# Performance work log

Measured on AMD Instinct MI355X. Metric: run time of the kernel, lower is better.

The kernel has to match this reference:

```python
import jax, jax.numpy as jnp
import numpy as np

B = 16384
EPS = 1e-5
DIMS = [(3072, 4096), (4096, 4096), (4096, 256), (256, 16), (16, 16), (16, 10)]


def binarize(v):
    # BNN binarization with straight-through semantics (matches .data assignment in torch)
    return v + jax.lax.stop_gradient(jnp.sign(v) - v)


def blinear(x, w, b):
    # BinarizeLinear: binarize input (in_dim != 784) and weights, float bias add
    return binarize(x) @ binarize(w).T + b


def batchnorm(x, g, b):
    m = x.mean(axis=0)
    v = x.var(axis=0)
    return (x - m) * jax.lax.rsqrt(v + EPS) * g + b


def hardtanh(x):
    return jnp.clip(x, -1.0, 1.0)


def setup_inputs() -> dict:
    key = jax.random.key(0)
    ks = jax.random.split(key, 20)
    inp = {"x": jax.random.normal(ks[0], (B, 3072), dtype=jnp.float32)}
    for i, (din, dout) in enumerate(DIMS):
        inp[f"w{i}"] = jax.random.normal(ks[1 + 2 * i], (dout, din), dtype=jnp.float32) * 0.05
        inp[f"b{i}"] = jax.random.normal(ks[2 + 2 * i], (dout,), dtype=jnp.float32) * 0.01
    # BatchNorm affine params for layers after blinear 0,1,2 and final (dims 4096,4096,256,10)
    for j, d in enumerate([4096, 4096, 256, 10]):
        inp[f"g{j}"] = jnp.ones((d,), dtype=jnp.float32)
        inp[f"be{j}"] = jnp.zeros((d,), dtype=jnp.float32)
    return inp


def reference(x, w0, b0, w1, b1, w2, b2, w3, b3, w4, b4, w5, b5,
              g0, be0, g1, be1, g2, be2, g3, be3):
    h = x.reshape(-1, 3072)
    h = hardtanh(batchnorm(blinear(h, w0, b0), g0, be0))
    h = hardtanh(batchnorm(blinear(h, w1, b1), g1, be1))
    h = hardtanh(batchnorm(blinear(h, w2, b2), g2, be2))
    h = hardtanh(blinear(h, w3, b3))
    h = hardtanh(blinear(h, w4, b4))
    h = batchnorm(blinear(h, w5, b5), g3, be3)
    return jax.nn.log_softmax(h, axis=-1)
```

## Files before the change

kernel.cpp:

```cpp
#include <hip/hip_runtime.h>
#include <stdint.h>

typedef int v4i __attribute__((ext_vector_type(4)));
typedef int v8i __attribute__((ext_vector_type(8)));
typedef float v4f __attribute__((ext_vector_type(4)));
typedef short v8s __attribute__((ext_vector_type(8)));
typedef unsigned long long ull;
typedef unsigned int uint;

#define GLOAD16(g, l)                                                          \
  __builtin_amdgcn_global_load_lds(                                            \
      (const __attribute__((address_space(1))) void*)(g),                      \
      (__attribute__((address_space(3))) void*)(l), 16, 0, 0)

__device__ __forceinline__ signed char sgnf(float v) {
  return v > 0.f ? (signed char)1 : (v < 0.f ? (signed char)-1 : (signed char)0);
}
__device__ __forceinline__ uint nib(float v) {
  return v > 0.f ? 2u : (v < 0.f ? 10u : 0u);
}

__global__ void k_bin(const float4* __restrict__ in, char4* __restrict__ out, int n4) {
  int i = blockIdx.x * blockDim.x + threadIdx.x;
  int stride = gridDim.x * blockDim.x;
  for (; i < n4; i += stride) {
    float4 v = in[i];
    char4 o;
    o.x = sgnf(v.x); o.y = sgnf(v.y); o.z = sgnf(v.z); o.w = sgnf(v.w);
    out[i] = o;
  }
}

__global__ void k_binp(const float4* __restrict__ in, uint* __restrict__ out, int n8) {
  int i = blockIdx.x * blockDim.x + threadIdx.x;
  int stride = gridDim.x * blockDim.x;
  for (; i < n8; i += stride) {
    float4 a = in[i * 2], b = in[i * 2 + 1];
    out[i] = nib(a.x) | (nib(a.y) << 4) | (nib(a.z) << 8) | (nib(a.w) << 12) |
             (nib(b.x) << 16) | (nib(b.y) << 20) | (nib(b.z) << 24) | (nib(b.w) << 28);
  }
}

#define BM 128
#define BN 128

__global__ __launch_bounds__(256, 2) void k_bgemm(
    const unsigned char* __restrict__ X, const unsigned char* __restrict__ W,
    short* __restrict__ A, ull* __restrict__ S, int M, int N, int K)
{
  __shared__ __align__(16) unsigned char As[BM * 128];
  __shared__ __align__(16) unsigned char Bs[BN * 128];
  const int Kb = K >> 1;
  const int t = threadIdx.x;
  const int lane = t & 63;
  const int wave = t >> 6;
  const int wm = wave >> 1, wn = wave & 1;
  const int bm = blockIdx.y * BM, bn = blockIdx.x * BN;

  const int srow = lane >> 3;
  const int sslot = (lane & 7);

  const unsigned char* Xb0 = X + (size_t)bm * Kb;
  const unsigned char* Wb0 = W + (size_t)bn * Kb;

  v4f acc[4][4] = {};
  v8i a8[4], b8[4];
#pragma unroll
  for (int m = 0; m < 4; ++m) { a8[m] = (v8i)(0); b8[m] = (v8i)(0); }

  const int nt = K / 256;

  for (int tile = 0; tile < nt; ++tile) {
    int kb0 = tile * 128;
#pragma unroll
    for (int c = 0; c < 4; ++c) {
      int br = (wave * 4 + c) * 8;
      int row = br + srow;
      int ss = sslot ^ (row & 7);
      GLOAD16(Xb0 + (size_t)row * Kb + kb0 + ss * 16, As + br * 128);
      GLOAD16(Wb0 + (size_t)row * Kb + kb0 + ss * 16, Bs + br * 128);
    }
    __syncthreads();
#pragma unroll
    for (int kk = 0; kk < 2; ++kk) {
#pragma unroll
      for (int m = 0; m < 4; ++m) {
        int row = wm * 64 + m * 16 + (lane & 15);
        int slot = ((kk << 2) | (lane >> 4)) ^ (row & 7);
        v4i tmp = *(const v4i*)(As + row * 128 + slot * 16);
        a8[m][0] = tmp[0]; a8[m][1] = tmp[1]; a8[m][2] = tmp[2]; a8[m][3] = tmp[3];
      }
#pragma unroll
      for (int n = 0; n < 4; ++n) {
        int row = wn * 64 + n * 16 + (lane & 15);
        int slot = ((kk << 2) | (lane >> 4)) ^ (row & 7);
        v4i tmp = *(const v4i*)(Bs + row * 128 + slot * 16);
        b8[n][0] = tmp[0]; b8[n][1] = tmp[1]; b8[n][2] = tmp[2]; b8[n][3] = tmp[3];
      }
#pragma unroll
      for (int m = 0; m < 4; ++m)
#pragma unroll
        for (int n = 0; n < 4; ++n)
          acc[m][n] = __builtin_amdgcn_mfma_scale_f32_16x16x128_f8f6f4(
              a8[m], b8[n], acc[m][n], 4 , 4 ,
              0, 0x7F7F7F7Fu, 0, 0x7F7F7F7Fu);
    }
    __syncthreads();
  }

#pragma unroll
  for (int m = 0; m < 4; ++m) {
    int rbase = bm + wm * 64 + m * 16 + (lane >> 4) * 4;
#pragma unroll
    for (int n = 0; n < 4; ++n) {
      int col = bn + wn * 64 + n * 16 + (lane & 15);
#pragma unroll
      for (int r = 0; r < 4; ++r)
        A[(size_t)(rbase + r) * N + col] = (short)(int)acc[m][n][r];
    }
  }

#pragma unroll
  for (int n = 0; n < 4; ++n) {
    int s = 0, q = 0;
#pragma unroll
    for (int m = 0; m < 4; ++m)
#pragma unroll
      for (int r = 0; r < 4; ++r) {
        int v = (int)acc[m][n][r];
        s += v; q += v * v;
      }
    s += __shfl_xor(s, 16); s += __shfl_xor(s, 32);
    q += __shfl_xor(q, 16); q += __shfl_xor(q, 32);
    if ((lane >> 4) == 0) {
      int col = bn + wn * 64 + n * 16 + (lane & 15);
      atomicAdd(&S[col], (ull)(long long)s);
      atomicAdd(&S[(size_t)N + col], (ull)(long long)q);
    }
  }
}

__global__ void k_finalize(const ull* __restrict__ sums, const float* __restrict__ g,
                           int M, int N, float* __restrict__ meanf, float* __restrict__ sgf) {
  int j = blockIdx.x * blockDim.x + threadIdx.x;
  if (j >= N) return;
  double sum = (double)(long long)sums[j];
  double sumsq = (double)(long long)sums[N + j];
  double mean = sum / (double)M;
  double var = sumsq / (double)M - mean * mean;
  if (var < 0.0) var = 0.0;
  double inv = 1.0 / sqrt(var + 1e-5);
  meanf[j] = (float)mean;
  sgf[j] = (float)(inv * (double)g[j]);
}

__global__ void k_signbn_pack(const short* __restrict__ A, const float* __restrict__ meanf,
                              const float* __restrict__ sgf, const float* __restrict__ be,
                              uint* __restrict__ Xp, int total8, int nmask) {
  int i = blockIdx.x * blockDim.x + threadIdx.x;
  int stride = gridDim.x * blockDim.x;
  for (; i < total8; i += stride) {
    v8s a = *(const v8s*)(A + (size_t)i * 8);
    int c0 = (i * 8) & nmask;
    uint b = 0;
#pragma unroll
    for (int j = 0; j < 8; ++j) {
      float z = ((float)a[j] - meanf[c0 + j]) * sgf[c0 + j] + be[c0 + j];
      b |= nib(z) << (4 * j);
    }
    Xp[i] = b;
  }
}

__global__ void k_signbn(const short4* __restrict__ A4, const float* __restrict__ meanf,
                         const float* __restrict__ sgf, const float* __restrict__ be,
                         char4* __restrict__ X4, int total4, int nmask) {
  int i = blockIdx.x * blockDim.x + threadIdx.x;
  int stride = gridDim.x * blockDim.x;
  for (; i < total4; i += stride) {
    short4 a = A4[i];
    int c0 = (i * 4) & nmask;
    char4 o;
    o.x = sgnf(((float)a.x - meanf[c0    ]) * sgf[c0    ] + be[c0    ]);
    o.y = sgnf(((float)a.y - meanf[c0 + 1]) * sgf[c0 + 1] + be[c0 + 1]);
    o.z = sgnf(((float)a.z - meanf[c0 + 2]) * sgf[c0 + 2] + be[c0 + 2]);
    o.w = sgnf(((float)a.w - meanf[c0 + 3]) * sgf[c0 + 3] + be[c0 + 3]);
    X4[i] = o;
  }
}

__global__ __launch_bounds__(256) void k_tail(
    const signed char* __restrict__ X3, const signed char* __restrict__ W3,
    const signed char* __restrict__ W4, const signed char* __restrict__ W5,
    const float* __restrict__ b3, const float* __restrict__ b4,
    int* __restrict__ A5, ull* __restrict__ sums5, int M)
{
  __shared__ __align__(16) signed char sW3[16 * 256];
  __shared__ __align__(16) signed char sW4[256];
  __shared__ __align__(16) signed char sW5[160];
  __shared__ __align__(16) signed char sX[16 * 256];
  __shared__ signed char sH[16][16];
  __shared__ int bsum[10], bsq[10];
  int t = threadIdx.x;
  int rowBlock = blockIdx.x * 16;
  ((int4*)sW3)[t] = ((const int4*)W3)[t];
  ((int4*)sX)[t] = ((const int4*)(X3 + (size_t)rowBlock * 256))[t];
  if (t < 16) ((int4*)sW4)[t] = ((const int4*)W4)[t];
  if (t < 10) {
    ((int4*)sW5)[t] = ((const int4*)W5)[t];
    bsum[t] = 0; bsq[t] = 0;
  }
  __syncthreads();
  int r = t >> 4, j = t & 15;
  int d3 = 0;
#pragma unroll 8
  for (int k = 0; k < 256; ++k) d3 += (int)sX[r * 256 + k] * (int)sW3[j * 256 + k];
  sH[r][j] = sgnf((float)d3 + b3[j]);
  __syncthreads();
  int d4 = 0;
#pragma unroll
  for (int k = 0; k < 16; ++k) d4 += (int)sH[r][k] * (int)sW4[j * 16 + k];
  signed char x5 = sgnf((float)d4 + b4[j]);
  __syncthreads();
  sH[r][j] = x5;
  __syncthreads();
  if (j < 10) {
    int d5 = 0;
#pragma unroll
    for (int k = 0; k < 16; ++k) d5 += (int)sH[r][k] * (int)sW5[j * 16 + k];
    A5[(size_t)(rowBlock + r) * 10 + j] = d5;
    atomicAdd(&bsum[j], d5);
    atomicAdd(&bsq[j], d5 * d5);
  }
  __syncthreads();
  if (t < 10) {
    atomicAdd(&sums5[t], (ull)(long long)bsum[t]);
    atomicAdd(&sums5[10 + t], (ull)(long long)bsq[t]);
  }
}

__global__ void k_lsm(const int* __restrict__ A5, const float* __restrict__ meanf,
                      const float* __restrict__ sgf, const float* __restrict__ be,
                      float* __restrict__ out, int M) {
  int r = blockIdx.x * blockDim.x + threadIdx.x;
  if (r >= M) return;
  float tv[10]; float mx = -3.0e38f;
#pragma unroll
  for (int j = 0; j < 10; ++j) {
    tv[j] = ((float)A5[(size_t)r * 10 + j] - meanf[j]) * sgf[j] + be[j];
    mx = fmaxf(mx, tv[j]);
  }
  float s = 0.f;
#pragma unroll
  for (int j = 0; j < 10; ++j) s += expf(tv[j] - mx);
  float lse = mx + logf(s);
#pragma unroll
  for (int j = 0; j < 10; ++j) out[(size_t)r * 10 + j] = tv[j] - lse;
}

extern "C" void kernel_launch(void* const* d_in, const int* in_sizes, int n_in,
                              void* d_out, int out_size, void* d_ws, size_t ws_size,
                              hipStream_t stream) {
  const float* x   = (const float*)d_in[0];
  const float* w0f = (const float*)d_in[1];
  const float* w1f = (const float*)d_in[3];
  const float* w2f = (const float*)d_in[5];
  const float* w3f = (const float*)d_in[7];  const float* b3f = (const float*)d_in[8];
  const float* w4f = (const float*)d_in[9];  const float* b4f = (const float*)d_in[10];
  const float* w5f = (const float*)d_in[11];
  const float* g0 = (const float*)d_in[13]; const float* be0 = (const float*)d_in[14];
  const float* g1 = (const float*)d_in[15]; const float* be1 = (const float*)d_in[16];
  const float* g2 = (const float*)d_in[17]; const float* be2 = (const float*)d_in[18];
  const float* g3 = (const float*)d_in[19]; const float* be3 = (const float*)d_in[20];

  const int M = in_sizes[0] / 3072;
  char* w = (char*)d_ws;
  short* Abuf          = (short*)w;
  unsigned char* X0p   = (unsigned char*)(w + 134217728);
  unsigned char* Xbp   = (unsigned char*)(w + 184549376);
  signed char* X3      = (signed char*)(w + 251658240);
  unsigned char* Ws0p  = (unsigned char*)(w + 255852544);
  unsigned char* Ws1p  = (unsigned char*)(w + 268435456);
  unsigned char* Ws2p  = (unsigned char*)(w + 285212672);
  signed char* Ws3 = (signed char*)(w + 286261248);
  signed char* Ws4 = (signed char*)(w + 286265344);
  signed char* Ws5 = (signed char*)(w + 286265600);
  int* A5          = (int*)(w + 286265856);
  ull* S0          = (ull*)(w + 286921216);
  ull* S1          = (ull*)(w + 286986752);
  ull* S2          = (ull*)(w + 287052288);
  ull* S5          = (ull*)(w + 287056384);
  float* P0m = (float*)(w + 287056640); float* P0s = (float*)(w + 287073024);
  float* P1m = (float*)(w + 287089408); float* P1s = (float*)(w + 287105792);
  float* P2m = (float*)(w + 287122176); float* P2s = (float*)(w + 287123200);
  float* P5m = (float*)(w + 287124224); float* P5s = (float*)(w + 287124288);

  hipMemsetAsync(w + 286921216, 0, 135424, stream);

  auto binp = [&](const float* src, unsigned char* dst, int n) {
    int n8 = n / 8;
    int grid = (n8 + 255) / 256; if (grid > 8192) grid = 8192;
    k_binp<<<grid, 256, 0, stream>>>((const float4*)src, (uint*)dst, n8);
  };
  binp(x,   X0p,  M * 3072);
  binp(w0f, Ws0p, 4096 * 3072);
  binp(w1f, Ws1p, 4096 * 4096);
  binp(w2f, Ws2p, 256 * 4096);
  k_bin<<<1, 64, 0, stream>>>((const float4*)w3f, (char4*)Ws3, 16 * 256 / 4);
  k_bin<<<1, 64, 0, stream>>>((const float4*)w4f, (char4*)Ws4, 16 * 16 / 4);
  k_bin<<<1, 40, 0, stream>>>((const float4*)w5f, (char4*)Ws5, 10 * 16 / 4);

  k_bgemm<<<dim3(4096 / BN, M / BM), 256, 0, stream>>>(X0p, Ws0p, Abuf, S0, M, 4096, 3072);
  k_finalize<<<16, 256, 0, stream>>>(S0, g0, M, 4096, P0m, P0s);
  k_signbn_pack<<<8192, 256, 0, stream>>>(Abuf, P0m, P0s, be0, (uint*)Xbp, M * 4096 / 8, 4095);

  k_bgemm<<<dim3(4096 / BN, M / BM), 256, 0, stream>>>(Xbp, Ws1p, Abuf, S1, M, 4096, 4096);
  k_finalize<<<16, 256, 0, stream>>>(S1, g1, M, 4096, P1m, P1s);
  k_signbn_pack<<<8192, 256, 0, stream>>>(Abuf, P1m, P1s, be1, (uint*)Xbp, M * 4096 / 8, 4095);

  k_bgemm<<<dim3(256 / BN, M / BM), 256, 0, stream>>>(Xbp, Ws2p, Abuf, S2, M, 256, 4096);
  k_finalize<<<1, 256, 0, stream>>>(S2, g2, M, 256, P2m, P2s);
  k_signbn<<<4096, 256, 0, stream>>>((const short4*)Abuf, P2m, P2s, be2, (char4*)X3, M * 256 / 4, 255);

  k_tail<<<M / 16, 256, 0, stream>>>(X3, Ws3, Ws4, Ws5, b3f, b4f, A5, S5, M);
  k_finalize<<<1, 32, 0, stream>>>(S5, g3, M, 10, P5m, P5s);
  k_lsm<<<(M + 255) / 256, 256, 0, stream>>>(A5, P5m, P5s, be3, (float*)d_out, M);

  (void)n_in; (void)out_size; (void)ws_size;
}
```

Before: 471.2 us.

## Template binary GEMM on K/N, remap workgroups across XCDs, precompute addresses

The binary GEMM kernel becomes a template on K and N, so the tile loop count and strides are compile-time constants and the K loop is fully unrolled. The 2D grid becomes a 1D grid, and block indices are remapped so that consecutive workgroups landing on the same XCD (round-robin over 8) cover neighbouring output tiles, which is meant to improve L2 reuse of the A and B panels. Global and LDS address arithmetic is hoisted out of the loop, and the inner loop uses XOR offsets. Full unrolling raises code size and may add register pressure, and the remap assumes the workgroup count divides evenly by 8.

```diff
diff --git a/kernel.cpp b/kernel.cpp
--- a/kernel.cpp
+++ b/kernel.cpp
@@ -44,18 +44,25 @@
 #define BM 128
 #define BN 128
 
+template <int K, int N>
 __global__ __launch_bounds__(256, 2) void k_bgemm(
     const unsigned char* __restrict__ X, const unsigned char* __restrict__ W,
-    short* __restrict__ A, ull* __restrict__ S, int M, int N, int K)
+    short* __restrict__ A, ull* __restrict__ S, int M)
 {
   __shared__ __align__(16) unsigned char As[BM * 128];
   __shared__ __align__(16) unsigned char Bs[BN * 128];
-  const int Kb = K >> 1;
+  constexpr int Kb = K >> 1;
+  constexpr int NT = K / 256;
+  constexpr int NBX = N / BN;
   const int t = threadIdx.x;
   const int lane = t & 63;
   const int wave = t >> 6;
   const int wm = wave >> 1, wn = wave & 1;
-  const int bm = blockIdx.y * BM, bn = blockIdx.x * BN;
+
+  const int nwg = gridDim.x;
+  const int lin = blockIdx.x;
+  const int wg = (lin & 7) * (nwg >> 3) + (lin >> 3);
+  const int bm = (wg / NBX) * BM, bn = (wg % NBX) * BN;
 
   const int srow = lane >> 3;
   const int sslot = (lane & 7);
@@ -68,33 +75,45 @@
 #pragma unroll
   for (int m = 0; m < 4; ++m) { a8[m] = (v8i)(0); b8[m] = (v8i)(0); }
 
-  const int nt = K / 256;
-
-  for (int tile = 0; tile < nt; ++tile) {
-    int kb0 = tile * 128;
+  const unsigned char* gx[4];
+  const unsigned char* gw[4];
+  int ldsoff[4];
+#pragma unroll
+  for (int c = 0; c < 4; ++c) {
+    int br = (wave * 4 + c) * 8;
+    int row = br + srow;
+    int ss = sslot ^ (row & 7);
+    gx[c] = Xb0 + (size_t)row * Kb + ss * 16;
+    gw[c] = Wb0 + (size_t)row * Kb + ss * 16;
+    ldsoff[c] = br * 128;
+  }
+  int aoff[4], boff[4];
+#pragma unroll
+  for (int m = 0; m < 4; ++m) {
+    int arow = wm * 64 + m * 16 + (lane & 15);
+    aoff[m] = arow * 128 + (((lane >> 4) ^ (arow & 7)) * 16);
+    int brow = wn * 64 + m * 16 + (lane & 15);
+    boff[m] = brow * 128 + (((lane >> 4) ^ (brow & 7)) * 16);
+  }
+
+#pragma unroll
+  for (int tile = 0; tile < NT; ++tile) {
 #pragma unroll
     for (int c = 0; c < 4; ++c) {
-      int br = (wave * 4 + c) * 8;
-      int row = br + srow;
-      int ss = sslot ^ (row & 7);
-      GLOAD16(Xb0 + (size_t)row * Kb + kb0 + ss * 16, As + br * 128);
-      GLOAD16(Wb0 + (size_t)row * Kb + kb0 + ss * 16, Bs + br * 128);
+      GLOAD16(gx[c] + tile * 128, As + ldsoff[c]);
+      GLOAD16(gw[c] + tile * 128, Bs + ldsoff[c]);
     }
     __syncthreads();
 #pragma unroll
     for (int kk = 0; kk < 2; ++kk) {
 #pragma unroll
       for (int m = 0; m < 4; ++m) {
-        int row = wm * 64 + m * 16 + (lane & 15);
-        int slot = ((kk << 2) | (lane >> 4)) ^ (row & 7);
-        v4i tmp = *(const v4i*)(As + row * 128 + slot * 16);
+        v4i tmp = *(const v4i*)(As + (aoff[m] ^ (kk << 6)));
         a8[m][0] = tmp[0]; a8[m][1] = tmp[1]; a8[m][2] = tmp[2]; a8[m][3] = tmp[3];
       }
 #pragma unroll
       for (int n = 0; n < 4; ++n) {
-        int row = wn * 64 + n * 16 + (lane & 15);
-        int slot = ((kk << 2) | (lane >> 4)) ^ (row & 7);
-        v4i tmp = *(const v4i*)(Bs + row * 128 + slot * 16);
+        v4i tmp = *(const v4i*)(Bs + (boff[n] ^ (kk << 6)));
         b8[n][0] = tmp[0]; b8[n][1] = tmp[1]; b8[n][2] = tmp[2]; b8[n][3] = tmp[3];
       }
 #pragma unroll
@@ -310,15 +329,15 @@
   k_bin<<<1, 64, 0, stream>>>((const float4*)w4f, (char4*)Ws4, 16 * 16 / 4);
   k_bin<<<1, 40, 0, stream>>>((const float4*)w5f, (char4*)Ws5, 10 * 16 / 4);
 
-  k_bgemm<<<dim3(4096 / BN, M / BM), 256, 0, stream>>>(X0p, Ws0p, Abuf, S0, M, 4096, 3072);
+  k_bgemm<3072, 4096><<<(4096 / BN) * (M / BM), 256, 0, stream>>>(X0p, Ws0p, Abuf, S0, M);
   k_finalize<<<16, 256, 0, stream>>>(S0, g0, M, 4096, P0m, P0s);
   k_signbn_pack<<<8192, 256, 0, stream>>>(Abuf, P0m, P0s, be0, (uint*)Xbp, M * 4096 / 8, 4095);
 
-  k_bgemm<<<dim3(4096 / BN, M / BM), 256, 0, stream>>>(Xbp, Ws1p, Abuf, S1, M, 4096, 4096);
+  k_bgemm<4096, 4096><<<(4096 / BN) * (M / BM), 256, 0, stream>>>(Xbp, Ws1p, Abuf, S1, M);
   k_finalize<<<16, 256, 0, stream>>>(S1, g1, M, 4096, P1m, P1s);
   k_signbn_pack<<<8192, 256, 0, stream>>>(Abuf, P1m, P1s, be1, (uint*)Xbp, M * 4096 / 8, 4095);
 
-  k_bgemm<<<dim3(256 / BN, M / BM), 256, 0, stream>>>(Xbp, Ws2p, Abuf, S2, M, 256, 4096);
+  k_bgemm<4096, 256><<<(256 / BN) * (M / BM), 256, 0, stream>>>(Xbp, Ws2p, Abuf, S2, M);
   k_finalize<<<1, 256, 0, stream>>>(S2, g2, M, 256, P2m, P2s);
   k_signbn<<<4096, 256, 0, stream>>>((const short4*)Abuf, P2m, P2s, be2, (char4*)X3, M * 256 / 4, 255);
 
```

Measured after the change: 522.9 us. 11.0% more time.
